# Optimization experiments

Measured on AMD Instinct MI355X. Metric: run time of the kernel, lower is better.

## Reference

```python
import jax, jax.numpy as jnp
import numpy as np

B, H, D = 32, 64, 512          # batch, attn heads, head_dim (shared KV: V == K cache)
ROPE = 64                       # qk_rope_head_dim (partial rotary on last 64 dims)
HALF = ROPE // 2
NB, BS = 2048, 64               # paged cache: num blocks, block size
MB = NB // B                    # blocks per sequence
SMAX = MB * BS                  # 4096 max cached tokens per sequence
IH, ID = 64, 128                # indexer heads / head dim
TOPK = 512                      # index_topk
SCALE = 1.0 / float(np.sqrt(D))


def partial_rotary(x, cos, sin):
    # interleaved rope on the LAST ROPE dims (rope_dim_start = D - ROPE)
    x1, x2 = x[..., :D - ROPE], x[..., D - ROPE:]
    c = cos[:, None, :]  # [B,1,HALF] broadcast over heads
    s = sin[:, None, :]
    xe, xo = x2[..., 0::2], x2[..., 1::2]
    re = xe * c - xo * s
    ro = xe * s + xo * c
    rot = jnp.stack([re, ro], axis=-1).reshape(x2.shape)
    return jnp.concatenate([x1, rot], axis=-1)


def dyn_quant(x):
    # per-token dynamic int8 quant (kept in f32; values are exact int8 levels)
    scale = jnp.maximum(jnp.max(jnp.abs(x), axis=-1, keepdims=True), 1e-12) / 127.0
    scale = jnp.where(scale < 1e-6, 1.0, scale)
    xq = jnp.clip(jnp.round(x / scale), -128.0, 127.0)
    return xq, scale


def setup_inputs() -> dict:
    key = jax.random.key(0)
    ks = jax.random.split(key, 8)
    q = jax.random.normal(ks[0], (B, H, D), jnp.float32)
    cos = jax.random.normal(ks[1], (B, HALF), jnp.float32)
    sin = jax.random.normal(ks[2], (B, HALF), jnp.float32)
    kv_cache = jax.random.normal(ks[3], (NB, BS, D), jnp.float32)
    q_idx = jax.random.normal(ks[4], (B, IH, ID), jnp.float32)
    k_idx_cache = jax.random.normal(ks[5], (NB, BS, ID), jnp.float32)
    attn_sink = jax.random.normal(ks[6], (H,), jnp.float32) * 0.1
    block_tables = jnp.arange(B * MB, dtype=jnp.int32).reshape(B, MB)
    seq_lens = jax.random.randint(ks[7], (B,), 2 * TOPK, SMAX + 1, dtype=jnp.int32)
    return dict(q=q, cos=cos, sin=sin, kv_cache=kv_cache, q_idx=q_idx,
                k_idx_cache=k_idx_cache, attn_sink=attn_sink,
                block_tables=block_tables, seq_lens=seq_lens)


def reference(q, cos, sin, kv_cache, q_idx, k_idx_cache, attn_sink, block_tables, seq_lens):
    # 1) partial interleaved rotary on q's last ROPE dims
    qr = partial_rotary(q, cos, sin)
    # 2) paged gather of shared KV and indexer K caches
    k_all = kv_cache[block_tables].reshape(B, SMAX, D)      # [B,S,D]
    k_idx = k_idx_cache[block_tables].reshape(B, SMAX, ID)  # [B,S,ID]
    pos = jnp.arange(SMAX)
    valid = pos[None, :] < seq_lens[:, None]                # [B,S]
    # 3) int8 lightning indexer -> top-k token selection
    qq, qs = dyn_quant(q_idx)                               # [B,IH,ID],[B,IH,1]
    kq, kss = dyn_quant(k_idx)                              # [B,S,ID],[B,S,1]
    iscore = (jnp.einsum('bhd,bsd->bhs', qq, kq) * qs).sum(axis=1) * kss[..., 0]  # [B,S]
    iscore = jnp.where(valid, iscore, -jnp.inf)
    _, top_idx = jax.lax.top_k(iscore, TOPK)                # [B,TOPK]
    sel = jnp.zeros((B, SMAX), bool).at[jnp.arange(B)[:, None], top_idx].set(True)
    keep = (sel & valid) | (pos[None, :] == 0)              # sink token always attended
    # 4) sparse shared-KV attention (V = K), attn_sink added on first cached token
    scores = jnp.einsum('bhd,bsd->bhs', qr, k_all) * SCALE
    scores = scores.at[:, :, 0].add(attn_sink[None, :])
    scores = jnp.where(keep[:, None, :], scores, -jnp.inf)
    w = jax.nn.softmax(scores, axis=-1)
    out = jnp.einsum('bhs,bsd->bhd', w, k_all)              # [B,H,D]
    return out
```

## Files before the change

kernel.cpp:

```cpp
#include <hip/hip_runtime.h>
#include <math.h>

#define B_ 32
#define H_ 64
#define D_ 512
#define ROPE_ 64
#define HALF_ 32
#define NB_ 2048
#define BS_ 64
#define MB_ 64
#define SMAX_ 4096
#define IH_ 64
#define ID_ 128
#define TOPK_ 512
#define SEL_CAP_ 544
#define KB_ROWS_ 576
#define SCALE_ 0.044194173824159216f

typedef __bf16 bf16x8 __attribute__((ext_vector_type(8)));
typedef float f32x4 __attribute__((ext_vector_type(4)));

__device__ __forceinline__ unsigned short f2bf(float f) {
  unsigned u = __float_as_uint(f);
  u += 0x7FFFu + ((u >> 16) & 1u);
  return (unsigned short)(u >> 16);
}

__global__ __launch_bounds__(64) void k_prep(
    const float* __restrict__ q, const float* __restrict__ cosb,
    const float* __restrict__ sinb, const float* __restrict__ q_idx,
    unsigned short* __restrict__ qrb, unsigned short* __restrict__ qqb,
    float* __restrict__ qs) {
  int r = blockIdx.x, t = threadIdx.x;
  if (r < B_ * H_) {
    const float* x = q + (size_t)r * D_;
    unsigned short* y = qrb + (size_t)r * D_;
    int b = r >> 6;
    unsigned pk[4];
    if (t < 56) {
      float4 v0 = ((const float4*)x)[t * 2];
      float4 v1 = ((const float4*)x)[t * 2 + 1];
      pk[0] = f2bf(v0.x) | ((unsigned)f2bf(v0.y) << 16);
      pk[1] = f2bf(v0.z) | ((unsigned)f2bf(v0.w) << 16);
      pk[2] = f2bf(v1.x) | ((unsigned)f2bf(v1.y) << 16);
      pk[3] = f2bf(v1.z) | ((unsigned)f2bf(v1.w) << 16);
      *(uint4*)(y + t * 8) = make_uint4(pk[0], pk[1], pk[2], pk[3]);
    } else {
      int p0 = (t - 56) * 4;
#pragma unroll
      for (int i = 0; i < 4; i++) {
        int p = p0 + i;
        float c = cosb[b * HALF_ + p], s = sinb[b * HALF_ + p];
        float xe = x[448 + 2 * p], xo = x[448 + 2 * p + 1];
        float re = xe * c - xo * s;
        float ro = xe * s + xo * c;
        pk[i] = f2bf(re) | ((unsigned)f2bf(ro) << 16);
      }
      *(uint4*)(y + 448 + 8 * (t - 56)) = make_uint4(pk[0], pk[1], pk[2], pk[3]);
    }
  } else {
    int rr = r - B_ * H_;
    const float* x = q_idx + (size_t)rr * ID_;
    float2 v = *(const float2*)(x + t * 2);
    float m = fmaxf(fabsf(v.x), fabsf(v.y));
#pragma unroll
    for (int off = 32; off; off >>= 1) m = fmaxf(m, __shfl_xor(m, off));
    float scale = fmaxf(m, 1e-12f) / 127.0f;
    if (scale < 1e-6f) scale = 1.0f;
    float q0 = fminf(fmaxf(rintf(v.x / scale), -128.0f), 127.0f);
    float q1 = fminf(fmaxf(rintf(v.y / scale), -128.0f), 127.0f);
    ((unsigned*)qqb)[rr * (ID_ / 2) + t] = f2bf(q0) | ((unsigned)f2bf(q1) << 16);
    if (t == 0) qs[rr] = scale;
  }
}

__global__ __launch_bounds__(256) void k_iscore(
    const float* __restrict__ k_idx_cache, const unsigned short* __restrict__ qqb,
    const float* __restrict__ qs, const int* __restrict__ block_tables,
    const int* __restrict__ seq_lens, float* __restrict__ iscore) {
  int m = blockIdx.x, b = blockIdx.y;
  int t = threadIdx.x, lane = t & 63, w = t >> 6;
  int s_base = m * BS_;
  int seq = seq_lens[b];
  float* out = iscore + (size_t)b * SMAX_ + s_base;
  if (s_base >= seq) {
    if (t < 64) out[t] = -INFINITY;
    return;
  }
  __shared__ __align__(16) unsigned short kq[64 * 136];
  __shared__ __align__(16) unsigned short qql[64 * 136];
  __shared__ float ksc[64];
  int phys = block_tables[b * MB_ + m];
  const float* krows = k_idx_cache + (size_t)phys * BS_ * ID_;
  int half = lane & 31, hw = lane >> 5;
  float4 vv[8];
#pragma unroll
  for (int rr = 0; rr < 8; rr++)
    vv[rr] = *(const float4*)(krows + (w * 16 + rr * 2 + hw) * ID_ + half * 4);
#pragma unroll
  for (int rr = 0; rr < 8; rr++) {
    int s = w * 16 + rr * 2 + hw;
    float4 v = vv[rr];
    float mx = fmaxf(fmaxf(fabsf(v.x), fabsf(v.y)), fmaxf(fabsf(v.z), fabsf(v.w)));
#pragma unroll
    for (int off = 1; off < 32; off <<= 1) mx = fmaxf(mx, __shfl_xor(mx, off));
    float scale = fmaxf(mx, 1e-12f) / 127.0f;
    if (scale < 1e-6f) scale = 1.0f;
    float q0 = fminf(fmaxf(rintf(v.x / scale), -128.0f), 127.0f);
    float q1 = fminf(fmaxf(rintf(v.y / scale), -128.0f), 127.0f);
    float q2 = fminf(fmaxf(rintf(v.z / scale), -128.0f), 127.0f);
    float q3 = fminf(fmaxf(rintf(v.w / scale), -128.0f), 127.0f);
    unsigned p0 = (unsigned)f2bf(q0) | ((unsigned)f2bf(q1) << 16);
    unsigned p1 = (unsigned)f2bf(q2) | ((unsigned)f2bf(q3) << 16);
    *(uint2*)((unsigned*)kq + s * 68 + half * 2) = make_uint2(p0, p1);
    if (half == 0) ksc[s] = scale;
  }
  const int4* qg = (const int4*)(qqb + (size_t)b * IH_ * ID_);
  for (int i = t; i < 64 * 16; i += 256) {
    int row = i >> 4, c = i & 15;
    *(int4*)((char*)qql + row * 272 + c * 16) = qg[row * 16 + c];
  }
  __syncthreads();
  int quad = lane >> 4, lr = lane & 15;
  float facc[4] = {0.f, 0.f, 0.f, 0.f};
  const float* qsrow = qs + b * IH_;
#pragma unroll
  for (int ht = 0; ht < 4; ht++) {
    f32x4 acc = {0.f, 0.f, 0.f, 0.f};
#pragma unroll
    for (int ks = 0; ks < 4; ks++) {
      bf16x8 a = *(const bf16x8*)(kq + (w * 16 + lr) * 136 + ks * 32 + quad * 8);
      bf16x8 bb = *(const bf16x8*)(qql + (ht * 16 + lr) * 136 + ks * 32 + quad * 8);
      acc = __builtin_amdgcn_mfma_f32_16x16x32_bf16(a, bb, acc, 0, 0, 0);
    }
    float qsv = qsrow[ht * 16 + lr];
#pragma unroll
    for (int r = 0; r < 4; r++) facc[r] += acc[r] * qsv;
  }
#pragma unroll
  for (int off = 1; off < 16; off <<= 1) {
#pragma unroll
    for (int r = 0; r < 4; r++) facc[r] += __shfl_xor(facc[r], off);
  }
  if (lr == 0) {
#pragma unroll
    for (int r = 0; r < 4; r++) {
      int sl = w * 16 + quad * 4 + r;
      out[sl] = (s_base + sl < seq) ? facc[r] * ksc[sl] : -INFINITY;
    }
  }
}

__global__ __launch_bounds__(256) void k_topk(
    const float* __restrict__ iscore, int* __restrict__ keep_idx,
    int* __restrict__ keep_cnt) {
  int b = blockIdx.x, t = threadIdx.x;
  int lane = t & 63, w = t >> 6;
  __shared__ unsigned keys[SMAX_];
  __shared__ unsigned hist[4][256];
  __shared__ unsigned wtot[4];
  __shared__ unsigned sh_prefix, sh_remaining, sh_cnt;
  const float* row = iscore + (size_t)b * SMAX_;
  for (int i = t; i < SMAX_; i += 256) {
    unsigned u = __float_as_uint(row[i]);
    keys[i] = (u & 0x80000000u) ? ~u : (u | 0x80000000u);
  }
  if (t == 0) { sh_prefix = 0u; sh_remaining = TOPK_; sh_cnt = 0u; }
  hist[0][t] = 0u; hist[1][t] = 0u; hist[2][t] = 0u; hist[3][t] = 0u;
  __syncthreads();
  for (int pass = 0; pass < 4; pass++) {
    int shift = 24 - 8 * pass;
    unsigned prefix = sh_prefix;
    unsigned rem = sh_remaining;
    unsigned pmask = (pass == 0) ? 0u : (0xFFFFFFFFu << (shift + 8));
    for (int i = t; i < SMAX_; i += 256) {
      unsigned k = keys[i];
      if ((k & pmask) == prefix) atomicAdd(&hist[w][(k >> shift) & 255u], 1u);
    }
    __syncthreads();
    unsigned cnt_t = hist[0][t] + hist[1][t] + hist[2][t] + hist[3][t];
    hist[0][t] = 0u; hist[1][t] = 0u; hist[2][t] = 0u; hist[3][t] = 0u;
    unsigned v = cnt_t;
#pragma unroll
    for (int off = 1; off < 64; off <<= 1) {
      unsigned o = __shfl_down(v, off);
      if (lane + off < 64) v += o;
    }
    if (lane == 0) wtot[w] = v;
    __syncthreads();
    unsigned tail = 0;
    for (int w2 = w + 1; w2 < 4; w2++) tail += wtot[w2];
    unsigned S = v + tail;
    if (S >= rem && S - cnt_t < rem) {
      sh_prefix = prefix | ((unsigned)t << shift);
      sh_remaining = rem - (S - cnt_t);
    }
    __syncthreads();
  }
  unsigned K = sh_prefix, R = sh_remaining;
  int* kidx = keep_idx + b * SEL_CAP_;
  for (int i = t; i < SMAX_; i += 256) {
    if (keys[i] > K) {
      unsigned p = atomicAdd(&sh_cnt, 1u);
      kidx[p] = i;
    }
  }
  int lo = t * 16;
  unsigned ec = 0;
#pragma unroll
  for (int j = 0; j < 16; j++) ec += (keys[lo + j] == K) ? 1u : 0u;
  unsigned pv = ec;
#pragma unroll
  for (int off = 1; off < 64; off <<= 1) {
    unsigned o = __shfl_up(pv, off);
    if (lane >= off) pv += o;
  }
  if (lane == 63) wtot[w] = pv;
  __syncthreads();
  unsigned base_eq = 0;
  for (int w2 = 0; w2 < w; w2++) base_eq += wtot[w2];
  unsigned rank = base_eq + pv - ec;
  unsigned G = sh_cnt;
  for (int j = 0; j < 16; j++) {
    if (keys[lo + j] == K) {
      if (rank < R) kidx[G + rank] = lo + j;
      rank++;
    }
  }
  __syncthreads();
  bool kept0 = (keys[0] >= K);
  int cnt = kept0 ? TOPK_ : (TOPK_ + 1);
  if (t == 0) {
    if (!kept0) kidx[TOPK_] = 0;
    keep_cnt[b] = cnt;
  }
  for (int i = cnt + t; i < SEL_CAP_; i += 256) kidx[i] = 0;
}

__global__ __launch_bounds__(256) void k_scores(
    const float* __restrict__ kv_cache, const unsigned short* __restrict__ qrb,
    const float* __restrict__ attn_sink, const int* __restrict__ block_tables,
    const int* __restrict__ keep_idx, const int* __restrict__ keep_cnt,
    float* __restrict__ scores, unsigned short* __restrict__ kb16) {
  int c = blockIdx.x, b = blockIdx.y;
  int t = threadIdx.x, lane = t & 63, w = t >> 6;
  int cnt = keep_cnt[b];
  int base = c * 64;
  int n = min(cnt - base, 64);
  if (n <= 0) return;
  __shared__ __align__(16) unsigned short kt[64 * 136];
  __shared__ __align__(16) unsigned short qt[64 * 136];
  __shared__ int srow_off[64];
  __shared__ int sglb[64];
  const int* kidx = keep_idx + b * SEL_CAP_;
  if (t < 64) {
    int sg = (t < n) ? kidx[base + t] : 0;
    sglb[t] = (t < n) ? sg : -1;
    srow_off[t] = block_tables[b * MB_ + (sg >> 6)] * BS_ + (sg & 63);
  }
  __syncthreads();
  int quad = lane >> 4, lr = lane & 15;
  f32x4 acc[4] = {};
  const int4* qg = (const int4*)qrb;
  for (int dr = 0; dr < 4; dr++) {
    __syncthreads();
    for (int i = t; i < 64 * 32; i += 256) {
      int row = i >> 5, d4 = i & 31;
      float4 v = {0.f, 0.f, 0.f, 0.f};
      if (row < n)
        v = *(const float4*)(kv_cache + (size_t)srow_off[row] * D_ + dr * 128 + d4 * 4);
      unsigned lo_ = f2bf(v.x) | ((unsigned)f2bf(v.y) << 16);
      unsigned hi_ = f2bf(v.z) | ((unsigned)f2bf(v.w) << 16);
      uint2 pk = make_uint2(lo_, hi_);
      *(uint2*)(kt + row * 136 + d4 * 4) = pk;
      *(uint2*)(kb16 + (size_t)(b * KB_ROWS_ + base + row) * D_ + dr * 128 + d4 * 4) = pk;
    }
    for (int i = t; i < 64 * 16; i += 256) {
      int row = i >> 4, cc = i & 15;
      *(int4*)((char*)qt + row * 272 + cc * 16) = qg[(size_t)(b * 64 + row) * 64 + dr * 16 + cc];
    }
    __syncthreads();
#pragma unroll
    for (int ks = 0; ks < 4; ks++) {
      bf16x8 a = *(const bf16x8*)(qt + (w * 16 + lr) * 136 + ks * 32 + quad * 8);
#pragma unroll
      for (int st = 0; st < 4; st++) {
        bf16x8 bb = *(const bf16x8*)(kt + (st * 16 + lr) * 136 + ks * 32 + quad * 8);
        acc[st] = __builtin_amdgcn_mfma_f32_16x16x32_bf16(a, bb, acc[st], 0, 0, 0);
      }
    }
  }
#pragma unroll
  for (int st = 0; st < 4; st++) {
    int col = st * 16 + lr;
    if (col < n) {
      int sg = sglb[col];
#pragma unroll
      for (int r = 0; r < 4; r++) {
        int h = w * 16 + quad * 4 + r;
        float v = acc[st][r] * SCALE_;
        if (sg == 0) v += attn_sink[h];
        scores[((size_t)b * 64 + h) * SEL_CAP_ + base + col] = v;
      }
    }
  }
}

__global__ __launch_bounds__(64) void k_softmax(
    const int* __restrict__ keep_cnt, float* __restrict__ scores,
    unsigned short* __restrict__ wbf) {
  int r = blockIdx.x, t = threadIdx.x;
  int b = r >> 6;
  int cnt = keep_cnt[b];
  float* row = scores + (size_t)r * SEL_CAP_;
  float mx = -INFINITY;
  for (int i = t; i < cnt; i += 64) mx = fmaxf(mx, row[i]);
#pragma unroll
  for (int off = 32; off; off >>= 1) mx = fmaxf(mx, __shfl_xor(mx, off));
  float sum = 0.f;
  for (int i = t; i < cnt; i += 64) {
    float e = __expf(row[i] - mx);
    row[i] = e;
    sum += e;
  }
#pragma unroll
  for (int off = 32; off; off >>= 1) sum += __shfl_xor(sum, off);
  float inv = 1.0f / sum;
  unsigned short* wr = wbf + (size_t)r * SEL_CAP_;
  for (int i = t; i < SEL_CAP_; i += 64) {
    float v = (i < cnt) ? row[i] * inv : 0.f;
    wr[i] = f2bf(v);
  }
}

__global__ __launch_bounds__(256) void k_pv(
    const unsigned short* __restrict__ kb16, const unsigned short* __restrict__ wbf,
    float* __restrict__ out) {
  int dc = blockIdx.x, b = blockIdx.y;
  int t = threadIdx.x, lane = t & 63, w = t >> 6;
  __shared__ __align__(16) unsigned short ktr[64 * 72];
  unsigned* kw = (unsigned*)ktr;
  int quad = lane >> 4, lr = lane & 15;
  f32x4 acc[4] = {};
  const unsigned short* kbb = kb16 + (size_t)b * KB_ROWS_ * D_ + dc * 64;
  const unsigned short* wrow = wbf + (size_t)(b * 64 + w * 16 + lr) * SEL_CAP_;
  for (int sc = 0; sc < 9; sc++) {
    int sbase = sc * 64;
    int width = (sc < 8) ? 64 : 32;
    __syncthreads();
    for (int i = t; i < (width >> 1) * 16; i += 256) {
      int sg2 = i >> 4, d4 = i & 15;
      int s0 = sbase + sg2 * 2;
      ushort4 a0 = *(const ushort4*)(kbb + (size_t)s0 * D_ + d4 * 4);
      ushort4 a1 = *(const ushort4*)(kbb + (size_t)(s0 + 1) * D_ + d4 * 4);
      kw[(d4 * 4 + 0) * 36 + sg2] = (unsigned)a0.x | ((unsigned)a1.x << 16);
      kw[(d4 * 4 + 1) * 36 + sg2] = (unsigned)a0.y | ((unsigned)a1.y << 16);
      kw[(d4 * 4 + 2) * 36 + sg2] = (unsigned)a0.z | ((unsigned)a1.z << 16);
      kw[(d4 * 4 + 3) * 36 + sg2] = (unsigned)a0.w | ((unsigned)a1.w << 16);
    }
    __syncthreads();
    int ksteps = width >> 5;
    for (int ks = 0; ks < ksteps; ks++) {
      bf16x8 a = *(const bf16x8*)(wrow + sbase + ks * 32 + quad * 8);
#pragma unroll
      for (int nt = 0; nt < 4; nt++) {
        int d = nt * 16 + lr;
        bf16x8 bb = *(const bf16x8*)(ktr + d * 72 + ks * 32 + quad * 8);
        acc[nt] = __builtin_amdgcn_mfma_f32_16x16x32_bf16(a, bb, acc[nt], 0, 0, 0);
      }
    }
  }
#pragma unroll
  for (int nt = 0; nt < 4; nt++) {
#pragma unroll
    for (int r = 0; r < 4; r++) {
      int h = w * 16 + quad * 4 + r;
      int d = dc * 64 + nt * 16 + lr;
      out[((size_t)b * 64 + h) * D_ + d] = acc[nt][r];
    }
  }
}

extern "C" void kernel_launch(void* const* d_in, const int* in_sizes, int n_in,
                              void* d_out, int out_size, void* d_ws, size_t ws_size,
                              hipStream_t stream) {
  (void)in_sizes; (void)n_in; (void)out_size; (void)ws_size;
  const float* q = (const float*)d_in[0];
  const float* cosb = (const float*)d_in[1];
  const float* sinb = (const float*)d_in[2];
  const float* kv_cache = (const float*)d_in[3];
  const float* q_idx = (const float*)d_in[4];
  const float* k_idx = (const float*)d_in[5];
  const float* sink = (const float*)d_in[6];
  const int* btab = (const int*)d_in[7];
  const int* slen = (const int*)d_in[8];
  float* out = (float*)d_out;
  char* ws = (char*)d_ws;
  unsigned short* qrb = (unsigned short*)(ws + 0);
  unsigned short* qqb = (unsigned short*)(ws + 2097152);
  float* qs = (float*)(ws + 2621440);
  float* iscore = (float*)(ws + 2629632);
  int* keep_idx = (int*)(ws + 3141632);
  int* keep_cnt = (int*)(ws + 3211264);
  float* scores = (float*)(ws + 3212288);
  unsigned short* wbf = (unsigned short*)(ws + 7668736);
  unsigned short* kb16 = (unsigned short*)(ws + 9896960);

  k_prep<<<dim3(4096), dim3(64), 0, stream>>>(q, cosb, sinb, q_idx, qrb, qqb, qs);
  k_iscore<<<dim3(64, 32), dim3(256), 0, stream>>>(k_idx, qqb, qs, btab, slen, iscore);
  k_topk<<<dim3(32), dim3(256), 0, stream>>>(iscore, keep_idx, keep_cnt);
  k_scores<<<dim3(9, 32), dim3(256), 0, stream>>>(kv_cache, qrb, sink, btab, keep_idx, keep_cnt, scores, kb16);
  k_softmax<<<dim3(2048), dim3(64), 0, stream>>>(keep_cnt, scores, wbf);
  k_pv<<<dim3(8, 32), dim3(256), 0, stream>>>(kb16, wbf, out);
}
```

Baseline: 427.1 us.

## Double-buffer K tiles and register-prefetch gathers in scores and PV kernels

k_scores now uses 32-row tiles over 17 blocks per batch, keeps the query fragments in registers instead of staging them in LDS, and register-prefetches the next 128-column slice of gathered KV while converting the current one into a double-buffered LDS tile. k_pv preloads all softmax weight fragments into registers and prefetches the next 64-token K chunk into registers while the current chunk is transposed into a double-buffered LDS tile. Both kernels use a single lgkmcnt wait plus barrier per stage instead of two __syncthreads. Empty tiles now zero their kb16 rows. The aim is to hide the latency of global gathers behind MFMA work and to add parallelism, at the cost of higher register pressure and more redundant query loads.

```diff
diff --git a/kernel.cpp b/kernel.cpp
--- a/kernel.cpp
+++ b/kernel.cpp
@@ -25,6 +25,12 @@
   u += 0x7FFFu + ((u >> 16) & 1u);
   return (unsigned short)(u >> 16);
 }
+
+#define BARSYNC()                                        \
+  do {                                                   \
+    asm volatile("s_waitcnt lgkmcnt(0)" ::: "memory");   \
+    __builtin_amdgcn_s_barrier();                        \
+  } while (0)
 
 __global__ __launch_bounds__(64) void k_prep(
     const float* __restrict__ q, const float* __restrict__ cosb,
@@ -245,53 +251,83 @@
   int c = blockIdx.x, b = blockIdx.y;
   int t = threadIdx.x, lane = t & 63, w = t >> 6;
   int cnt = keep_cnt[b];
-  int base = c * 64;
-  int n = min(cnt - base, 64);
-  if (n <= 0) return;
-  __shared__ __align__(16) unsigned short kt[64 * 136];
-  __shared__ __align__(16) unsigned short qt[64 * 136];
-  __shared__ int srow_off[64];
-  __shared__ int sglb[64];
+  int base = c * 32;
+  int n = min(cnt - base, 32);
+  unsigned short* kbrow = kb16 + (size_t)(b * KB_ROWS_ + base) * D_;
+  if (n <= 0) {
+    for (int i = t; i < 32 * 32; i += 256) {
+      int row = i >> 5, x = i & 31;
+      *(uint4*)(kbrow + (size_t)row * D_ + x * 16) = make_uint4(0u, 0u, 0u, 0u);
+    }
+    return;
+  }
+  __shared__ __align__(16) unsigned short kt[2][32 * 136];
+  __shared__ int srow_off[32];
+  __shared__ int sglb[32];
   const int* kidx = keep_idx + b * SEL_CAP_;
-  if (t < 64) {
+  if (t < 32) {
     int sg = (t < n) ? kidx[base + t] : 0;
     sglb[t] = (t < n) ? sg : -1;
     srow_off[t] = block_tables[b * MB_ + (sg >> 6)] * BS_ + (sg & 63);
   }
+  int quad = lane >> 4, lr = lane & 15;
+  bf16x8 qa[4][4];
+  {
+    const unsigned short* qrow = qrb + (size_t)(b * 64 + w * 16 + lr) * D_ + quad * 8;
+#pragma unroll
+    for (int dr = 0; dr < 4; dr++)
+#pragma unroll
+      for (int ks = 0; ks < 4; ks++)
+        qa[dr][ks] = *(const bf16x8*)(qrow + dr * 128 + ks * 32);
+  }
   __syncthreads();
-  int quad = lane >> 4, lr = lane & 15;
-  f32x4 acc[4] = {};
-  const int4* qg = (const int4*)qrb;
+  int prow = t >> 5, pd4 = t & 31;
+  float4 pvA[4], pvB[4];
+#pragma unroll
+  for (int it = 0; it < 4; it++) {
+    int row = prow + it * 8;
+    pvA[it] = make_float4(0.f, 0.f, 0.f, 0.f);
+    if (row < n)
+      pvA[it] = *(const float4*)(kv_cache + (size_t)srow_off[row] * D_ + pd4 * 4);
+  }
+  f32x4 acc[2] = {};
+#pragma unroll
   for (int dr = 0; dr < 4; dr++) {
-    __syncthreads();
-    for (int i = t; i < 64 * 32; i += 256) {
-      int row = i >> 5, d4 = i & 31;
-      float4 v = {0.f, 0.f, 0.f, 0.f};
-      if (row < n)
-        v = *(const float4*)(kv_cache + (size_t)srow_off[row] * D_ + dr * 128 + d4 * 4);
+    if (dr < 3) {
+#pragma unroll
+      for (int it = 0; it < 4; it++) {
+        int row = prow + it * 8;
+        pvB[it] = make_float4(0.f, 0.f, 0.f, 0.f);
+        if (row < n)
+          pvB[it] = *(const float4*)(kv_cache + (size_t)srow_off[row] * D_ +
+                                     (dr + 1) * 128 + pd4 * 4);
+      }
+    }
+    unsigned short* ktc = kt[dr & 1];
+#pragma unroll
+    for (int it = 0; it < 4; it++) {
+      int row = prow + it * 8;
+      float4 v = pvA[it];
       unsigned lo_ = f2bf(v.x) | ((unsigned)f2bf(v.y) << 16);
       unsigned hi_ = f2bf(v.z) | ((unsigned)f2bf(v.w) << 16);
       uint2 pk = make_uint2(lo_, hi_);
-      *(uint2*)(kt + row * 136 + d4 * 4) = pk;
-      *(uint2*)(kb16 + (size_t)(b * KB_ROWS_ + base + row) * D_ + dr * 128 + d4 * 4) = pk;
-    }
-    for (int i = t; i < 64 * 16; i += 256) {
-      int row = i >> 4, cc = i & 15;
-      *(int4*)((char*)qt + row * 272 + cc * 16) = qg[(size_t)(b * 64 + row) * 64 + dr * 16 + cc];
-    }
-    __syncthreads();
+      *(uint2*)(ktc + row * 136 + pd4 * 4) = pk;
+      *(uint2*)(kbrow + (size_t)row * D_ + dr * 128 + pd4 * 4) = pk;
+    }
+    BARSYNC();
 #pragma unroll
     for (int ks = 0; ks < 4; ks++) {
-      bf16x8 a = *(const bf16x8*)(qt + (w * 16 + lr) * 136 + ks * 32 + quad * 8);
-#pragma unroll
-      for (int st = 0; st < 4; st++) {
-        bf16x8 bb = *(const bf16x8*)(kt + (st * 16 + lr) * 136 + ks * 32 + quad * 8);
-        acc[st] = __builtin_amdgcn_mfma_f32_16x16x32_bf16(a, bb, acc[st], 0, 0, 0);
-      }
-    }
-  }
-#pragma unroll
-  for (int st = 0; st < 4; st++) {
+#pragma unroll
+      for (int st = 0; st < 2; st++) {
+        bf16x8 bb = *(const bf16x8*)(ktc + (st * 16 + lr) * 136 + ks * 32 + quad * 8);
+        acc[st] = __builtin_amdgcn_mfma_f32_16x16x32_bf16(qa[dr][ks], bb, acc[st], 0, 0, 0);
+      }
+    }
+#pragma unroll
+    for (int it = 0; it < 4; it++) pvA[it] = pvB[it];
+  }
+#pragma unroll
+  for (int st = 0; st < 2; st++) {
     int col = st * 16 + lr;
     if (col < n) {
       int sg = sglb[col];
@@ -338,37 +374,66 @@
     float* __restrict__ out) {
   int dc = blockIdx.x, b = blockIdx.y;
   int t = threadIdx.x, lane = t & 63, w = t >> 6;
-  __shared__ __align__(16) unsigned short ktr[64 * 72];
-  unsigned* kw = (unsigned*)ktr;
+  __shared__ __align__(16) unsigned short ktr[2][64 * 72];
   int quad = lane >> 4, lr = lane & 15;
   f32x4 acc[4] = {};
   const unsigned short* kbb = kb16 + (size_t)b * KB_ROWS_ * D_ + dc * 64;
   const unsigned short* wrow = wbf + (size_t)(b * 64 + w * 16 + lr) * SEL_CAP_;
+  bf16x8 wa[17];
+#pragma unroll
+  for (int j = 0; j < 17; j++) wa[j] = *(const bf16x8*)(wrow + j * 32 + quad * 8);
+  int psg2 = t >> 4, pd4 = t & 15;
+  ushort4 paA[2][2], paB[2][2];
+#pragma unroll
+  for (int it = 0; it < 2; it++) {
+    int sg2 = psg2 + it * 16;
+    int s0 = sg2 * 2;
+    paA[it][0] = *(const ushort4*)(kbb + (size_t)s0 * D_ + pd4 * 4);
+    paA[it][1] = *(const ushort4*)(kbb + (size_t)(s0 + 1) * D_ + pd4 * 4);
+  }
+#pragma unroll
   for (int sc = 0; sc < 9; sc++) {
-    int sbase = sc * 64;
     int width = (sc < 8) ? 64 : 32;
-    __syncthreads();
-    for (int i = t; i < (width >> 1) * 16; i += 256) {
-      int sg2 = i >> 4, d4 = i & 15;
-      int s0 = sbase + sg2 * 2;
-      ushort4 a0 = *(const ushort4*)(kbb + (size_t)s0 * D_ + d4 * 4);
-      ushort4 a1 = *(const ushort4*)(kbb + (size_t)(s0 + 1) * D_ + d4 * 4);
-      kw[(d4 * 4 + 0) * 36 + sg2] = (unsigned)a0.x | ((unsigned)a1.x << 16);
-      kw[(d4 * 4 + 1) * 36 + sg2] = (unsigned)a0.y | ((unsigned)a1.y << 16);
-      kw[(d4 * 4 + 2) * 36 + sg2] = (unsigned)a0.z | ((unsigned)a1.z << 16);
-      kw[(d4 * 4 + 3) * 36 + sg2] = (unsigned)a0.w | ((unsigned)a1.w << 16);
-    }
-    __syncthreads();
+    if (sc < 8) {
+      int nw = ((sc + 1) < 8) ? 64 : 32;
+#pragma unroll
+      for (int it = 0; it < 2; it++) {
+        int sg2 = psg2 + it * 16;
+        if (sg2 < (nw >> 1)) {
+          int s0 = (sc + 1) * 64 + sg2 * 2;
+          paB[it][0] = *(const ushort4*)(kbb + (size_t)s0 * D_ + pd4 * 4);
+          paB[it][1] = *(const ushort4*)(kbb + (size_t)(s0 + 1) * D_ + pd4 * 4);
+        }
+      }
+    }
+    unsigned* kw = (unsigned*)ktr[sc & 1];
+#pragma unroll
+    for (int it = 0; it < 2; it++) {
+      int sg2 = psg2 + it * 16;
+      if (sg2 < (width >> 1)) {
+        ushort4 a0 = paA[it][0], a1 = paA[it][1];
+        kw[(pd4 * 4 + 0) * 36 + sg2] = (unsigned)a0.x | ((unsigned)a1.x << 16);
+        kw[(pd4 * 4 + 1) * 36 + sg2] = (unsigned)a0.y | ((unsigned)a1.y << 16);
+        kw[(pd4 * 4 + 2) * 36 + sg2] = (unsigned)a0.z | ((unsigned)a1.z << 16);
+        kw[(pd4 * 4 + 3) * 36 + sg2] = (unsigned)a0.w | ((unsigned)a1.w << 16);
+      }
+    }
+    BARSYNC();
+    const unsigned short* ktc = ktr[sc & 1];
     int ksteps = width >> 5;
-    for (int ks = 0; ks < ksteps; ks++) {
-      bf16x8 a = *(const bf16x8*)(wrow + sbase + ks * 32 + quad * 8);
-#pragma unroll
-      for (int nt = 0; nt < 4; nt++) {
-        int d = nt * 16 + lr;
-        bf16x8 bb = *(const bf16x8*)(ktr + d * 72 + ks * 32 + quad * 8);
-        acc[nt] = __builtin_amdgcn_mfma_f32_16x16x32_bf16(a, bb, acc[nt], 0, 0, 0);
-      }
-    }
+#pragma unroll
+    for (int ks = 0; ks < 2; ks++) {
+      if (ks < ksteps) {
+        bf16x8 a = wa[sc * 2 + ks];
+#pragma unroll
+        for (int nt = 0; nt < 4; nt++) {
+          bf16x8 bb = *(const bf16x8*)(ktc + (nt * 16 + lr) * 72 + ks * 32 + quad * 8);
+          acc[nt] = __builtin_amdgcn_mfma_f32_16x16x32_bf16(a, bb, acc[nt], 0, 0, 0);
+        }
+      }
+    }
+#pragma unroll
+    for (int it = 0; it < 2; it++) { paA[it][0] = paB[it][0]; paA[it][1] = paB[it][1]; }
   }
 #pragma unroll
   for (int nt = 0; nt < 4; nt++) {
@@ -409,7 +474,7 @@
   k_prep<<<dim3(4096), dim3(64), 0, stream>>>(q, cosb, sinb, q_idx, qrb, qqb, qs);
   k_iscore<<<dim3(64, 32), dim3(256), 0, stream>>>(k_idx, qqb, qs, btab, slen, iscore);
   k_topk<<<dim3(32), dim3(256), 0, stream>>>(iscore, keep_idx, keep_cnt);
-  k_scores<<<dim3(9, 32), dim3(256), 0, stream>>>(kv_cache, qrb, sink, btab, keep_idx, keep_cnt, scores, kb16);
+  k_scores<<<dim3(17, 32), dim3(256), 0, stream>>>(kv_cache, qrb, sink, btab, keep_idx, keep_cnt, scores, kb16);
   k_softmax<<<dim3(2048), dim3(64), 0, stream>>>(keep_cnt, scores, wbf);
   k_pv<<<dim3(8, 32), dim3(256), 0, stream>>>(kb16, wbf, out);
 }
```

New measurement: 403.6 us. 5.5% less time.
